# Kernel optimization log

Hardware: AMD Instinct MI355X
Metric: run time of the kernel (lower is better)

## Reference

```python
import jax, jax.numpy as jnp
import numpy as np

B1, B2 = 4096, 4096
DF, MF = 1024, 512
H1, H2, H3, H1_ = 2048, 1024, 512, 1024
DO, MO = 1, 1


def _lin(x, W, b):
    return x @ W.T + b


def setup_inputs() -> dict:
    key = jax.random.key(0)
    ks = jax.random.split(key, 22)

    def w(k, o, i):
        return (jax.random.normal(k, (o, i), jnp.float32) / np.sqrt(i)).astype(jnp.float32)

    def bz(k, o):
        return jax.random.normal(k, (o,), jnp.float32) * 0.01

    return {
        'x1': jax.random.normal(ks[0], (B1, DF), jnp.float32),
        'x2': jax.random.normal(ks[1], (B2, MF), jnp.float32),
        'W1_1': w(ks[2], H1, DF),  'b1_1': bz(ks[3], H1),
        'W1_2': w(ks[4], H2, H1),  'b1_2': bz(ks[5], H2),
        'W1_3': w(ks[6], H3, H2),  'b1_3': bz(ks[7], H3),
        'W1_4': w(ks[8], H2, H3),  'b1_4': bz(ks[9], H2),
        'W1_5': w(ks[10], H1, H2), 'b1_5': bz(ks[11], H1),
        'Wp1':  w(ks[12], DO, H1), 'bp1':  bz(ks[13], DO),
        'W2_1': w(ks[14], H1_, MF), 'b2_1': bz(ks[15], H1_),
        'W2_2': w(ks[16], H3, H1_), 'b2_2': bz(ks[17], H3),
        'W2_3': w(ks[18], H1_, H3), 'b2_3': bz(ks[19], H1_),
        'Wp2':  w(ks[20], MO, H1_), 'bp2':  bz(ks[21], MO),
    }


def reference(x1, x2, W1_1, b1_1, W1_2, b1_2, W1_3, b1_3, W1_4, b1_4,
              W1_5, b1_5, Wp1, bp1, W2_1, b2_1, W2_2, b2_2, W2_3, b2_3,
              Wp2, bp2):
    # dropout: eval mode (identity)
    h = jax.nn.relu(_lin(x1, W1_1, b1_1))
    h = jax.nn.relu(_lin(h, W1_2, b1_2))
    x_1 = jax.nn.sigmoid(_lin(h, W1_3, b1_3))          # [B1, H3]
    h = jax.nn.relu(_lin(x_1, W1_4, b1_4))
    h = jax.nn.relu(_lin(h, W1_5, b1_5))
    x2_1 = jax.nn.sigmoid(_lin(h, Wp1, bp1))           # [B1, DO]

    g = jax.nn.relu(_lin(x2, W2_1, b2_1))
    x_2 = jax.nn.sigmoid(_lin(g, W2_2, b2_2))          # [B2, H3]
    g = jax.nn.relu(_lin(x_2, W2_3, b2_3))
    x2_2 = jax.nn.sigmoid(_lin(g, Wp2, bp2))           # [B2, MO]

    # Python loop over x_1 rows doing (x_2 * row).sum(1) == single GEMM x_1 @ x_2.T
    scores = x_1 @ x_2.T                                # [B1, B2]
    pre_dm = scores.reshape(-1)                         # row-major matches torch.cat order
    # MinMaxScaler.fit_transform on detached values (original uses .data -> no grad)
    pre_dm = jax.lax.stop_gradient(pre_dm)
    mn, mx = pre_dm.min(), pre_dm.max()
    pre_dm = (pre_dm - mn) / (mx - mn)

    pre_data = x2_1.reshape(-1)
    pre_model = x2_2.T.reshape(-1)
    return (pre_data, pre_dm, pre_model)
```

## Files before the change

### kernel.cpp

```cpp
#include <hip/hip_runtime.h>
#include <hip/hip_bf16.h>

typedef __bf16 bf16_t;
typedef bf16_t bf16x8 __attribute__((ext_vector_type(8)));
typedef bf16_t bf16x4 __attribute__((ext_vector_type(4)));
typedef float f32x4 __attribute__((ext_vector_type(4)));

typedef __attribute__((address_space(1))) const void gconst_void;
typedef __attribute__((address_space(3))) void lds_void;

__device__ __forceinline__ void async16(const bf16_t* g, bf16_t* l) {
  __builtin_amdgcn_global_load_lds((gconst_void*)g, (lds_void*)l, 16, 0, 0);
}

struct CvtDesc { const float* src; bf16_t* dst; long n; };
struct CvtArgs { CvtDesc d[10]; };

__global__ __launch_bounds__(256) void cvt_many(CvtArgs a) {
  const CvtDesc de = a.d[blockIdx.y];
  long i = ((long)blockIdx.x * 256 + threadIdx.x) * 4;
  const long stride = (long)gridDim.x * 256 * 4;
  for (; i < de.n; i += stride) {
    float4 v = *(const float4*)(de.src + i);
    bf16x4 o;
    o[0] = (bf16_t)v.x; o[1] = (bf16_t)v.y; o[2] = (bf16_t)v.z; o[3] = (bf16_t)v.w;
    *(bf16x4*)(de.dst + i) = o;
  }
}

template <int ACT, bool HAS_BIAS, typename OutT>
__global__ __launch_bounds__(256) void gemm_bt(
    const bf16_t* __restrict__ A, const bf16_t* __restrict__ W,
    const float* __restrict__ bias, OutT* __restrict__ C,
    int M, int N, int K) {
  __shared__ __align__(16) bf16_t As[128 * 32];
  __shared__ __align__(16) bf16_t Bs[128 * 32];

  const int t = threadIdx.x;
  const int wave = t >> 6;
  const int lane = t & 63;
  const int quad = lane >> 4;
  const int l15 = lane & 15;

  const int bm = blockIdx.x * 128;
  const int bn = blockIdx.y * 128;
  const int wm = (wave >> 1) * 64;
  const int wn = (wave & 1) * 64;

  f32x4 acc[4][4];
#pragma unroll
  for (int i = 0; i < 4; ++i)
#pragma unroll
    for (int j = 0; j < 4; ++j) acc[i][j] = (f32x4){0.f, 0.f, 0.f, 0.f};

  const int c0 = t, c1 = t + 256;
  const long ga0 = (long)(bm + (c0 >> 2)) * K + (c0 & 3) * 8;
  const long ga1 = (long)(bm + (c1 >> 2)) * K + (c1 & 3) * 8;
  const long gb0 = (long)(bn + (c0 >> 2)) * K + (c0 & 3) * 8;
  const long gb1 = (long)(bn + (c1 >> 2)) * K + (c1 & 3) * 8;
  bf16_t* lA0 = As + c0 * 8;
  bf16_t* lA1 = As + c1 * 8;
  bf16_t* lB0 = Bs + c0 * 8;
  bf16_t* lB1 = Bs + c1 * 8;

  for (int k0 = 0; k0 < K; k0 += 32) {
    __syncthreads();
    async16(A + ga0 + k0, lA0);
    async16(A + ga1 + k0, lA1);
    async16(W + gb0 + k0, lB0);
    async16(W + gb1 + k0, lB1);
    __syncthreads();

    bf16x8 af[4], bfr[4];
#pragma unroll
    for (int i = 0; i < 4; ++i)
      af[i] = *(const bf16x8*)&As[(wm + i * 16 + l15) * 32 + quad * 8];
#pragma unroll
    for (int j = 0; j < 4; ++j)
      bfr[j] = *(const bf16x8*)&Bs[(wn + j * 16 + l15) * 32 + quad * 8];
#pragma unroll
    for (int i = 0; i < 4; ++i)
#pragma unroll
      for (int j = 0; j < 4; ++j)
        acc[i][j] = __builtin_amdgcn_mfma_f32_16x16x32_bf16(af[i], bfr[j],
                                                            acc[i][j], 0, 0, 0);
  }

  const int row0 = bm + wm + quad * 4;
  const int col0 = bn + wn + l15;
#pragma unroll
  for (int j = 0; j < 4; ++j) {
    const int col = col0 + j * 16;
    float bv = 0.f;
    if (HAS_BIAS) bv = bias[col];
#pragma unroll
    for (int i = 0; i < 4; ++i) {
#pragma unroll
      for (int r = 0; r < 4; ++r) {
        float v = acc[i][j][r] + bv;
        if (ACT == 1) v = fmaxf(v, 0.f);
        if (ACT == 2) v = 1.f / (1.f + expf(-v));
        C[(long)(row0 + i * 16 + r) * N + col] = (OutT)v;
      }
    }
  }
}

__global__ __launch_bounds__(64) void rowdot_sig(
    const bf16_t* __restrict__ A, const float* __restrict__ w,
    const float* __restrict__ b, float* __restrict__ out, int K) {
  const int row = blockIdx.x;
  const int lane = threadIdx.x;
  const bf16_t* a = A + (long)row * K;
  float s = 0.f;
  for (int k = lane * 8; k < K; k += 64 * 8) {
    bf16x8 av = *(const bf16x8*)&a[k];
    float4 w0 = *(const float4*)&w[k];
    float4 w1 = *(const float4*)&w[k + 4];
    s += (float)av[0] * w0.x + (float)av[1] * w0.y +
         (float)av[2] * w0.z + (float)av[3] * w0.w +
         (float)av[4] * w1.x + (float)av[5] * w1.y +
         (float)av[6] * w1.z + (float)av[7] * w1.w;
  }
#pragma unroll
  for (int off = 32; off > 0; off >>= 1) s += __shfl_down(s, off);
  if (lane == 0) {
    float v = s + b[0];
    out[row] = 1.f / (1.f + expf(-v));
  }
}

__global__ __launch_bounds__(256) void minmax_part(
    const float* __restrict__ s, long n, float* __restrict__ pmin,
    float* __restrict__ pmax) {
  long i = ((long)blockIdx.x * 256 + threadIdx.x) * 4;
  const long stride = (long)gridDim.x * 256 * 4;
  float mn = 3.4e38f, mx = -3.4e38f;
  for (; i < n; i += stride) {
    float4 v = *(const float4*)&s[i];
    mn = fminf(mn, fminf(fminf(v.x, v.y), fminf(v.z, v.w)));
    mx = fmaxf(mx, fmaxf(fmaxf(v.x, v.y), fmaxf(v.z, v.w)));
  }
#pragma unroll
  for (int off = 32; off > 0; off >>= 1) {
    mn = fminf(mn, __shfl_down(mn, off));
    mx = fmaxf(mx, __shfl_down(mx, off));
  }
  __shared__ float smn[4], smx[4];
  const int wv = threadIdx.x >> 6, ln = threadIdx.x & 63;
  if (ln == 0) { smn[wv] = mn; smx[wv] = mx; }
  __syncthreads();
  if (threadIdx.x == 0) {
    pmin[blockIdx.x] = fminf(fminf(smn[0], smn[1]), fminf(smn[2], smn[3]));
    pmax[blockIdx.x] = fmaxf(fmaxf(smx[0], smx[1]), fmaxf(smx[2], smx[3]));
  }
}

__global__ __launch_bounds__(256) void minmax_final(
    const float* __restrict__ pmin, const float* __restrict__ pmax, int nb,
    float* __restrict__ res) {
  float mn = 3.4e38f, mx = -3.4e38f;
  for (int i = threadIdx.x; i < nb; i += 256) {
    mn = fminf(mn, pmin[i]);
    mx = fmaxf(mx, pmax[i]);
  }
#pragma unroll
  for (int off = 32; off > 0; off >>= 1) {
    mn = fminf(mn, __shfl_down(mn, off));
    mx = fmaxf(mx, __shfl_down(mx, off));
  }
  __shared__ float smn[4], smx[4];
  const int wv = threadIdx.x >> 6, ln = threadIdx.x & 63;
  if (ln == 0) { smn[wv] = mn; smx[wv] = mx; }
  __syncthreads();
  if (threadIdx.x == 0) {
    float m0 = fminf(fminf(smn[0], smn[1]), fminf(smn[2], smn[3]));
    float m1 = fmaxf(fmaxf(smx[0], smx[1]), fmaxf(smx[2], smx[3]));
    res[0] = m0;
    res[1] = 1.f / (m1 - m0);
  }
}

__global__ __launch_bounds__(256) void normalize_k(
    float* __restrict__ out, const float* __restrict__ res, long n) {
  const float mn = res[0], inv = res[1];
  long i = ((long)blockIdx.x * 256 + threadIdx.x) * 4;
  const long stride = (long)gridDim.x * 256 * 4;
  for (; i < n; i += stride) {
    float4 v = *(const float4*)&out[i];
    v.x = (v.x - mn) * inv;
    v.y = (v.y - mn) * inv;
    v.z = (v.z - mn) * inv;
    v.w = (v.w - mn) * inv;
    *(float4*)&out[i] = v;
  }
}

extern "C" void kernel_launch(void* const* d_in, const int* in_sizes, int n_in,
                              void* d_out, int out_size, void* d_ws,
                              size_t ws_size, hipStream_t stream) {
  const float* x1   = (const float*)d_in[0];
  const float* x2   = (const float*)d_in[1];
  const float* W1_1 = (const float*)d_in[2];   const float* b1_1 = (const float*)d_in[3];
  const float* W1_2 = (const float*)d_in[4];   const float* b1_2 = (const float*)d_in[5];
  const float* W1_3 = (const float*)d_in[6];   const float* b1_3 = (const float*)d_in[7];
  const float* W1_4 = (const float*)d_in[8];   const float* b1_4 = (const float*)d_in[9];
  const float* W1_5 = (const float*)d_in[10];  const float* b1_5 = (const float*)d_in[11];
  const float* Wp1  = (const float*)d_in[12];  const float* bp1  = (const float*)d_in[13];
  const float* W2_1 = (const float*)d_in[14];  const float* b2_1 = (const float*)d_in[15];
  const float* W2_2 = (const float*)d_in[16];  const float* b2_2 = (const float*)d_in[17];
  const float* W2_3 = (const float*)d_in[18];  const float* b2_3 = (const float*)d_in[19];
  const float* Wp2  = (const float*)d_in[20];  const float* bp2  = (const float*)d_in[21];

  float* out = (float*)d_out;
  float* out_pre_data  = out;
  float* out_pre_dm    = out + 4096;
  float* out_pre_model = out + 4096 + (long)4096 * 4096;

  char* arena = (char*)out_pre_dm;
  const size_t MB = 1024 * 1024;
  bf16_t* x1b   = (bf16_t*)(arena);
  bf16_t* x2b   = (bf16_t*)(arena + 8 * MB);
  bf16_t* W1_1b = (bf16_t*)(arena + 12 * MB);
  bf16_t* W1_2b = (bf16_t*)(arena + 16 * MB);
  bf16_t* W1_3b = (bf16_t*)(arena + 20 * MB);
  bf16_t* W1_4b = (bf16_t*)(arena + 21 * MB);
  bf16_t* W1_5b = (bf16_t*)(arena + 22 * MB);
  bf16_t* W2_1b = (bf16_t*)(arena + 26 * MB);
  bf16_t* W2_2b = (bf16_t*)(arena + 27 * MB);
  bf16_t* W2_3b = (bf16_t*)(arena + 28 * MB);
  bf16_t* bufA  = (bf16_t*)(arena + 32 * MB);
  bf16_t* bufB  = (bf16_t*)(arena + 48 * MB);

  char* ws = (char*)d_ws;
  bf16_t* bufX1 = (bf16_t*)(ws);
  bf16_t* bufX2 = (bf16_t*)(ws + 4 * MB);
  float* pmin = (float*)(ws + 8 * MB);
  float* pmax = pmin + 1024;
  float* res  = pmax + 1024;

  CvtArgs ca;
  ca.d[0] = {x1,   x1b,   (long)4096 * 1024};
  ca.d[1] = {x2,   x2b,   (long)4096 * 512};
  ca.d[2] = {W1_1, W1_1b, (long)2048 * 1024};
  ca.d[3] = {W1_2, W1_2b, (long)1024 * 2048};
  ca.d[4] = {W1_3, W1_3b, (long)512 * 1024};
  ca.d[5] = {W1_4, W1_4b, (long)1024 * 512};
  ca.d[6] = {W1_5, W1_5b, (long)2048 * 1024};
  ca.d[7] = {W2_1, W2_1b, (long)1024 * 512};
  ca.d[8] = {W2_2, W2_2b, (long)512 * 1024};
  ca.d[9] = {W2_3, W2_3b, (long)1024 * 512};

  const dim3 blk(256);
  const long nS = (long)4096 * 4096;

  cvt_many<<<dim3(128, 10), blk, 0, stream>>>(ca);

  gemm_bt<1, true, bf16_t><<<dim3(32, 16), blk, 0, stream>>>(x1b, W1_1b, b1_1, bufA, 4096, 2048, 1024);
  gemm_bt<1, true, bf16_t><<<dim3(32, 8),  blk, 0, stream>>>(bufA, W1_2b, b1_2, bufB, 4096, 1024, 2048);
  gemm_bt<2, true, bf16_t><<<dim3(32, 4),  blk, 0, stream>>>(bufB, W1_3b, b1_3, bufX1, 4096, 512, 1024);
  gemm_bt<1, true, bf16_t><<<dim3(32, 8),  blk, 0, stream>>>(bufX1, W1_4b, b1_4, bufB, 4096, 1024, 512);
  gemm_bt<1, true, bf16_t><<<dim3(32, 16), blk, 0, stream>>>(bufB, W1_5b, b1_5, bufA, 4096, 2048, 1024);
  rowdot_sig<<<4096, 64, 0, stream>>>(bufA, Wp1, bp1, out_pre_data, 2048);

  gemm_bt<1, true, bf16_t><<<dim3(32, 8), blk, 0, stream>>>(x2b, W2_1b, b2_1, bufB, 4096, 1024, 512);
  gemm_bt<2, true, bf16_t><<<dim3(32, 4), blk, 0, stream>>>(bufB, W2_2b, b2_2, bufX2, 4096, 512, 1024);
  gemm_bt<1, true, bf16_t><<<dim3(32, 8), blk, 0, stream>>>(bufX2, W2_3b, b2_3, bufB, 4096, 1024, 512);
  rowdot_sig<<<4096, 64, 0, stream>>>(bufB, Wp2, bp2, out_pre_model, 1024);

  gemm_bt<0, false, float><<<dim3(32, 32), blk, 0, stream>>>(bufX1, bufX2, nullptr, out_pre_dm, 4096, 4096, 512);
  minmax_part<<<1024, blk, 0, stream>>>(out_pre_dm, nS, pmin, pmax);
  minmax_final<<<1, blk, 0, stream>>>(pmin, pmax, 1024, res);
  normalize_k<<<1024, blk, 0, stream>>>(out_pre_dm, res, nS);
}
```

Before: 424.4 us.

## Batch both MLP branches into grouped GEMMs, double-buffer LDS, fuse minmax into scores GEMM

Replaces the per-layer GEMM kernel with a grouped GEMM that runs the two independent MLP branches in the same launch. The K-loop now prefetches the next tile into a second LDS buffer, and LDS chunks are stored with a row-rotated swizzle to cut bank conflicts. The scores GEMM computes per-block min/max in its epilogue, so the separate full pass over the 64MB score matrix is dropped. The two rowdot kernels are merged into one launch, and grid sizes change for the convert and normalize kernels. The cost is runtime branching on the activation and bias inside the epilogue, plus twice the LDS per block.

After: 360.5 us. -15.1%, faster.

```diff
diff --git a/kernel.cpp b/kernel.cpp
--- a/kernel.cpp
+++ b/kernel.cpp
@@ -28,22 +28,31 @@
   }
 }
 
-template <int ACT, bool HAS_BIAS, typename OutT>
-__global__ __launch_bounds__(256) void gemm_bt(
-    const bf16_t* __restrict__ A, const bf16_t* __restrict__ W,
-    const float* __restrict__ bias, OutT* __restrict__ C,
-    int M, int N, int K) {
-  __shared__ __align__(16) bf16_t As[128 * 32];
-  __shared__ __align__(16) bf16_t Bs[128 * 32];
+struct GDesc {
+  const bf16_t* A; const bf16_t* W; const float* bias; void* C;
+  int N, K, act;
+};
+struct GArgs { GDesc d[2]; int ntiles0; };
+
+template <typename OutT, bool MINMAX>
+__global__ __launch_bounds__(256) void gemm_gb(GArgs ga, float* __restrict__ pmin,
+                                               float* __restrict__ pmax) {
+  const int b = blockIdx.x;
+  const int p = (b >= ga.ntiles0) ? 1 : 0;
+  const GDesc d = ga.d[p];
+  const int local = b - (p ? ga.ntiles0 : 0);
+  const int bm = (local & 31) * 128;
+  const int bn = (local >> 5) * 128;
+  const int N = d.N, K = d.K;
+
+  __shared__ __align__(16) bf16_t As[2][128 * 32];
+  __shared__ __align__(16) bf16_t Bs[2][128 * 32];
 
   const int t = threadIdx.x;
   const int wave = t >> 6;
   const int lane = t & 63;
   const int quad = lane >> 4;
   const int l15 = lane & 15;
-
-  const int bm = blockIdx.x * 128;
-  const int bn = blockIdx.y * 128;
   const int wm = (wave >> 1) * 64;
   const int wn = (wave & 1) * 64;
 
@@ -54,69 +63,98 @@
     for (int j = 0; j < 4; ++j) acc[i][j] = (f32x4){0.f, 0.f, 0.f, 0.f};
 
   const int c0 = t, c1 = t + 256;
-  const long ga0 = (long)(bm + (c0 >> 2)) * K + (c0 & 3) * 8;
-  const long ga1 = (long)(bm + (c1 >> 2)) * K + (c1 & 3) * 8;
-  const long gb0 = (long)(bn + (c0 >> 2)) * K + (c0 & 3) * 8;
-  const long gb1 = (long)(bn + (c1 >> 2)) * K + (c1 & 3) * 8;
-  bf16_t* lA0 = As + c0 * 8;
-  bf16_t* lA1 = As + c1 * 8;
-  bf16_t* lB0 = Bs + c0 * 8;
-  bf16_t* lB1 = Bs + c1 * 8;
-
+  const int r0 = c0 >> 2, kc0 = ((c0 & 3) - r0) & 3;
+  const int r1 = c1 >> 2, kc1 = ((c1 & 3) - r1) & 3;
+  const bf16_t* pa0 = d.A + (long)(bm + r0) * K + kc0 * 8;
+  const bf16_t* pa1 = d.A + (long)(bm + r1) * K + kc1 * 8;
+  const bf16_t* pw0 = d.W + (long)(bn + r0) * K + kc0 * 8;
+  const bf16_t* pw1 = d.W + (long)(bn + r1) * K + kc1 * 8;
+  bf16_t* lA0 = &As[0][c0 * 8]; bf16_t* lA1 = &As[0][c1 * 8];
+  bf16_t* lB0 = &Bs[0][c0 * 8]; bf16_t* lB1 = &Bs[0][c1 * 8];
+  const int bufOff = 128 * 32;
+
+  async16(pa0, lA0); async16(pa1, lA1);
+  async16(pw0, lB0); async16(pw1, lB1);
+
+  int buf = 0;
   for (int k0 = 0; k0 < K; k0 += 32) {
     __syncthreads();
-    async16(A + ga0 + k0, lA0);
-    async16(A + ga1 + k0, lA1);
-    async16(W + gb0 + k0, lB0);
-    async16(W + gb1 + k0, lB1);
-    __syncthreads();
-
+    const int kn = k0 + 32;
+    if (kn < K) {
+      const int o = (buf ^ 1) * bufOff;
+      async16(pa0 + kn, lA0 + o); async16(pa1 + kn, lA1 + o);
+      async16(pw0 + kn, lB0 + o); async16(pw1 + kn, lB1 + o);
+    }
+    const bf16_t* as = As[buf];
+    const bf16_t* bs = Bs[buf];
     bf16x8 af[4], bfr[4];
 #pragma unroll
-    for (int i = 0; i < 4; ++i)
-      af[i] = *(const bf16x8*)&As[(wm + i * 16 + l15) * 32 + quad * 8];
-#pragma unroll
-    for (int j = 0; j < 4; ++j)
-      bfr[j] = *(const bf16x8*)&Bs[(wn + j * 16 + l15) * 32 + quad * 8];
+    for (int i = 0; i < 4; ++i) {
+      const int r = wm + i * 16 + l15;
+      af[i] = *(const bf16x8*)&as[r * 32 + ((quad + r) & 3) * 8];
+    }
+#pragma unroll
+    for (int j = 0; j < 4; ++j) {
+      const int r = wn + j * 16 + l15;
+      bfr[j] = *(const bf16x8*)&bs[r * 32 + ((quad + r) & 3) * 8];
+    }
 #pragma unroll
     for (int i = 0; i < 4; ++i)
 #pragma unroll
       for (int j = 0; j < 4; ++j)
         acc[i][j] = __builtin_amdgcn_mfma_f32_16x16x32_bf16(af[i], bfr[j],
                                                             acc[i][j], 0, 0, 0);
-  }
-
+    buf ^= 1;
+  }
+
+  OutT* C = (OutT*)d.C;
   const int row0 = bm + wm + quad * 4;
   const int col0 = bn + wn + l15;
+  float mn = 3.4e38f, mx = -3.4e38f;
 #pragma unroll
   for (int j = 0; j < 4; ++j) {
     const int col = col0 + j * 16;
-    float bv = 0.f;
-    if (HAS_BIAS) bv = bias[col];
+    const float bv = d.bias ? d.bias[col] : 0.f;
 #pragma unroll
     for (int i = 0; i < 4; ++i) {
 #pragma unroll
       for (int r = 0; r < 4; ++r) {
         float v = acc[i][j][r] + bv;
-        if (ACT == 1) v = fmaxf(v, 0.f);
-        if (ACT == 2) v = 1.f / (1.f + expf(-v));
+        if (d.act == 1) v = fmaxf(v, 0.f);
+        else if (d.act == 2) v = 1.f / (1.f + expf(-v));
         C[(long)(row0 + i * 16 + r) * N + col] = (OutT)v;
+        if (MINMAX) { mn = fminf(mn, v); mx = fmaxf(mx, v); }
       }
     }
   }
-}
-
-__global__ __launch_bounds__(64) void rowdot_sig(
-    const bf16_t* __restrict__ A, const float* __restrict__ w,
-    const float* __restrict__ b, float* __restrict__ out, int K) {
+  if (MINMAX) {
+#pragma unroll
+    for (int off = 32; off > 0; off >>= 1) {
+      mn = fminf(mn, __shfl_down(mn, off));
+      mx = fmaxf(mx, __shfl_down(mx, off));
+    }
+    __shared__ float smn[4], smx[4];
+    if (lane == 0) { smn[wave] = mn; smx[wave] = mx; }
+    __syncthreads();
+    if (t == 0) {
+      pmin[blockIdx.x] = fminf(fminf(smn[0], smn[1]), fminf(smn[2], smn[3]));
+      pmax[blockIdx.x] = fmaxf(fmaxf(smx[0], smx[1]), fmaxf(smx[2], smx[3]));
+    }
+  }
+}
+
+struct RDesc { const bf16_t* A; const float* w; const float* b; float* out; int K; };
+
+__global__ __launch_bounds__(64) void rowdot2(RDesc d0, RDesc d1) {
+  const RDesc d = blockIdx.y ? d1 : d0;
   const int row = blockIdx.x;
   const int lane = threadIdx.x;
-  const bf16_t* a = A + (long)row * K;
+  const bf16_t* a = d.A + (long)row * d.K;
   float s = 0.f;
-  for (int k = lane * 8; k < K; k += 64 * 8) {
+  for (int k = lane * 8; k < d.K; k += 64 * 8) {
     bf16x8 av = *(const bf16x8*)&a[k];
-    float4 w0 = *(const float4*)&w[k];
-    float4 w1 = *(const float4*)&w[k + 4];
+    float4 w0 = *(const float4*)&d.w[k];
+    float4 w1 = *(const float4*)&d.w[k + 4];
     s += (float)av[0] * w0.x + (float)av[1] * w0.y +
          (float)av[2] * w0.z + (float)av[3] * w0.w +
          (float)av[4] * w1.x + (float)av[5] * w1.y +
@@ -124,36 +162,7 @@
   }
 #pragma unroll
   for (int off = 32; off > 0; off >>= 1) s += __shfl_down(s, off);
-  if (lane == 0) {
-    float v = s + b[0];
-    out[row] = 1.f / (1.f + expf(-v));
-  }
-}
-
-__global__ __launch_bounds__(256) void minmax_part(
-    const float* __restrict__ s, long n, float* __restrict__ pmin,
-    float* __restrict__ pmax) {
-  long i = ((long)blockIdx.x * 256 + threadIdx.x) * 4;
-  const long stride = (long)gridDim.x * 256 * 4;
-  float mn = 3.4e38f, mx = -3.4e38f;
-  for (; i < n; i += stride) {
-    float4 v = *(const float4*)&s[i];
-    mn = fminf(mn, fminf(fminf(v.x, v.y), fminf(v.z, v.w)));
-    mx = fmaxf(mx, fmaxf(fmaxf(v.x, v.y), fmaxf(v.z, v.w)));
-  }
-#pragma unroll
-  for (int off = 32; off > 0; off >>= 1) {
-    mn = fminf(mn, __shfl_down(mn, off));
-    mx = fmaxf(mx, __shfl_down(mx, off));
-  }
-  __shared__ float smn[4], smx[4];
-  const int wv = threadIdx.x >> 6, ln = threadIdx.x & 63;
-  if (ln == 0) { smn[wv] = mn; smx[wv] = mx; }
-  __syncthreads();
-  if (threadIdx.x == 0) {
-    pmin[blockIdx.x] = fminf(fminf(smn[0], smn[1]), fminf(smn[2], smn[3]));
-    pmax[blockIdx.x] = fmaxf(fmaxf(smx[0], smx[1]), fmaxf(smx[2], smx[3]));
-  }
+  if (lane == 0) d.out[row] = 1.f / (1.f + expf(-(s + d.b[0])));
 }
 
 __global__ __launch_bounds__(256) void minmax_final(
@@ -231,6 +240,7 @@
   bf16_t* W2_3b = (bf16_t*)(arena + 28 * MB);
   bf16_t* bufA  = (bf16_t*)(arena + 32 * MB);
   bf16_t* bufB  = (bf16_t*)(arena + 48 * MB);
+  bf16_t* bufC  = (bf16_t*)(arena + 56 * MB);
 
   char* ws = (char*)d_ws;
   bf16_t* bufX1 = (bf16_t*)(ws);
@@ -250,26 +260,45 @@
   ca.d[7] = {W2_1, W2_1b, (long)1024 * 512};
   ca.d[8] = {W2_2, W2_2b, (long)512 * 1024};
   ca.d[9] = {W2_3, W2_3b, (long)1024 * 512};
-
-  const dim3 blk(256);
+  cvt_many<<<dim3(192, 10), 256, 0, stream>>>(ca);
+
   const long nS = (long)4096 * 4096;
-
-  cvt_many<<<dim3(128, 10), blk, 0, stream>>>(ca);
-
-  gemm_bt<1, true, bf16_t><<<dim3(32, 16), blk, 0, stream>>>(x1b, W1_1b, b1_1, bufA, 4096, 2048, 1024);
-  gemm_bt<1, true, bf16_t><<<dim3(32, 8),  blk, 0, stream>>>(bufA, W1_2b, b1_2, bufB, 4096, 1024, 2048);
-  gemm_bt<2, true, bf16_t><<<dim3(32, 4),  blk, 0, stream>>>(bufB, W1_3b, b1_3, bufX1, 4096, 512, 1024);
-  gemm_bt<1, true, bf16_t><<<dim3(32, 8),  blk, 0, stream>>>(bufX1, W1_4b, b1_4, bufB, 4096, 1024, 512);
-  gemm_bt<1, true, bf16_t><<<dim3(32, 16), blk, 0, stream>>>(bufB, W1_5b, b1_5, bufA, 4096, 2048, 1024);
-  rowdot_sig<<<4096, 64, 0, stream>>>(bufA, Wp1, bp1, out_pre_data, 2048);
-
-  gemm_bt<1, true, bf16_t><<<dim3(32, 8), blk, 0, stream>>>(x2b, W2_1b, b2_1, bufB, 4096, 1024, 512);
-  gemm_bt<2, true, bf16_t><<<dim3(32, 4), blk, 0, stream>>>(bufB, W2_2b, b2_2, bufX2, 4096, 512, 1024);
-  gemm_bt<1, true, bf16_t><<<dim3(32, 8), blk, 0, stream>>>(bufX2, W2_3b, b2_3, bufB, 4096, 1024, 512);
-  rowdot_sig<<<4096, 64, 0, stream>>>(bufB, Wp2, bp2, out_pre_model, 1024);
-
-  gemm_bt<0, false, float><<<dim3(32, 32), blk, 0, stream>>>(bufX1, bufX2, nullptr, out_pre_dm, 4096, 4096, 512);
-  minmax_part<<<1024, blk, 0, stream>>>(out_pre_dm, nS, pmin, pmax);
-  minmax_final<<<1, blk, 0, stream>>>(pmin, pmax, 1024, res);
-  normalize_k<<<1024, blk, 0, stream>>>(out_pre_dm, res, nS);
-}
+  GArgs g;
+
+  g.d[0] = {x1b, W1_1b, b1_1, bufA, 2048, 1024, 1};
+  g.d[1] = {x2b, W2_1b, b2_1, bufC, 1024, 512, 1};
+  g.ntiles0 = 512;
+  gemm_gb<bf16_t, false><<<768, 256, 0, stream>>>(g, nullptr, nullptr);
+
+  g.d[0] = {bufA, W1_2b, b1_2, bufB, 1024, 2048, 1};
+  g.d[1] = {bufC, W2_2b, b2_2, bufX2, 512, 1024, 2};
+  g.ntiles0 = 256;
+  gemm_gb<bf16_t, false><<<384, 256, 0, stream>>>(g, nullptr, nullptr);
+
+  g.d[0] = {bufB, W1_3b, b1_3, bufX1, 512, 1024, 2};
+  g.d[1] = {bufX2, W2_3b, b2_3, bufC, 1024, 512, 1};
+  g.ntiles0 = 128;
+  gemm_gb<bf16_t, false><<<384, 256, 0, stream>>>(g, nullptr, nullptr);
+
+  g.d[0] = {bufX1, W1_4b, b1_4, bufB, 1024, 512, 1};
+  g.d[1] = g.d[0];
+  g.ntiles0 = 256;
+  gemm_gb<bf16_t, false><<<256, 256, 0, stream>>>(g, nullptr, nullptr);
+
+  g.d[0] = {bufB, W1_5b, b1_5, bufA, 2048, 1024, 1};
+  g.d[1] = g.d[0];
+  g.ntiles0 = 512;
+  gemm_gb<bf16_t, false><<<512, 256, 0, stream>>>(g, nullptr, nullptr);
+
+  RDesc r0 = {bufA, Wp1, bp1, out_pre_data, 2048};
+  RDesc r1 = {bufC, Wp2, bp2, out_pre_model, 1024};
+  rowdot2<<<dim3(4096, 2), 64, 0, stream>>>(r0, r1);
+
+  g.d[0] = {bufX1, bufX2, nullptr, out_pre_dm, 4096, 512, 0};
+  g.d[1] = g.d[0];
+  g.ntiles0 = 1024;
+  gemm_gb<float, true><<<1024, 256, 0, stream>>>(g, pmin, pmax);
+
+  minmax_final<<<1, 256, 0, stream>>>(pmin, pmax, 1024, res);
+  normalize_k<<<2048, 256, 0, stream>>>(out_pre_dm, res, nS);
+}
```
